# Optimization experiments

Measured on AMD Instinct MI355X. Metric: run time of the kernel, lower is better.

The kernel has to match this reference:

```python
import jax, jax.numpy as jnp
import numpy as np
import math

C = 512
D = C // 4  # 128
SCALE = math.sqrt(D)

def setup_inputs() -> dict:
    key = jax.random.key(0)
    k1, k2, k3, k4 = jax.random.split(key, 4)
    x = jax.random.normal(k1, (8, C, 2048), dtype=jnp.float32)
    # q_conv and k_conv share the same weight (tied in the torch module)
    wqk = jax.random.normal(k2, (D, C), dtype=jnp.float32) * (1.0 / math.sqrt(C))
    wv = jax.random.normal(k3, (D, C), dtype=jnp.float32) * (1.0 / math.sqrt(C))
    bv = jax.random.normal(k4, (D,), dtype=jnp.float32) * 0.01
    return {"x": x, "wqk": wqk, "wv": wv, "bv": bv}

def reference(x, wqk, wv, bv):
    # x: [B, C, N]; 1x1 conv == matmul over channel dim
    xq = jnp.einsum('dc,bcn->bnd', wqk, x)          # [B, N, D]
    xk = jnp.einsum('dc,bcn->bdn', wqk, x)          # [B, D, N]
    xv = jnp.einsum('dc,bcn->bdn', wv, x) + bv[None, :, None]  # [B, D, N]
    energy = jnp.einsum('bnd,bdm->bnm', xq, xk) / SCALE  # [B, N, N]
    attention = jax.nn.softmax(energy, axis=-1)
    x_r = jnp.einsum('bdn,bnm->bdm', xv, attention)  # [B, D, N]
    return x_r
```

## Files before the change

kernel.cpp:

```cpp
#include <hip/hip_runtime.h>

typedef short short4v __attribute__((ext_vector_type(4)));
typedef short short8 __attribute__((ext_vector_type(8)));
typedef float floatx4 __attribute__((ext_vector_type(4)));
typedef unsigned int uint;
typedef unsigned short ushort;

#define CH 512
#define NN 2048
#define DD 128
#define RSCALE 0.08838834764831845f

__device__ __forceinline__ float bf2f(ushort u) {
    union { uint i; float f; } v; v.i = ((uint)u) << 16; return v.f;
}
__device__ __forceinline__ ushort f2bf(float f) {
    union { float f; uint u; } v; v.f = f;
    uint u = v.u;
    return (ushort)((u + 0x7fffu + ((u >> 16) & 1u)) >> 16);
}

__global__ __launch_bounds__(256) void k0_prep(
    const float* __restrict__ wqk, const float* __restrict__ wv,
    ushort* __restrict__ Wbf, float* __restrict__ lsum,
    float* __restrict__ out)
{
    int gid = blockIdx.x * 256 + threadIdx.x;
    float4 z; z.x = 0.f; z.y = 0.f; z.z = 0.f; z.w = 0.f;
    *(float4*)&out[gid * 4] = z;
    if (gid < 32768) {
        int base = gid * 4;
        const float* src = (base < 65536) ? (wqk + base) : (wv + base - 65536);
        float4 v = *(const float4*)src;
        short4v o;
        o[0] = (short)f2bf(v.x); o[1] = (short)f2bf(v.y);
        o[2] = (short)f2bf(v.z); o[3] = (short)f2bf(v.w);
        *(short4v*)&Wbf[base] = o;
    }
    if (gid < 16384) lsum[gid] = 0.0f;
}

__global__ __launch_bounds__(256) void k1_proj(
    const float* __restrict__ x,
    const ushort* __restrict__ Wbf,
    const float* __restrict__ bv,
    ushort* __restrict__ Q,
    ushort* __restrict__ VT)
{
    const int nt = blockIdx.x;
    const int b  = blockIdx.y;
    const int n0 = nt * 32;
    const int t = threadIdx.x;
    const int lane = t & 63, w = t >> 6, l15 = lane & 15, quad = lane >> 4;

    __shared__ __attribute__((aligned(16))) ushort As[32 * 40];
    __shared__ __attribute__((aligned(16))) ushort Bs[256 * 40];
    __shared__ __attribute__((aligned(16))) ushort Vt[128 * 40];

    floatx4 acc[2][4];
#pragma unroll
    for (int i = 0; i < 2; i++)
#pragma unroll
        for (int j = 0; j < 4; j++) acc[i][j] = (floatx4)(0.0f);

    const float* xb = x + b * (CH * NN) + n0;

    for (int c0 = 0; c0 < CH; c0 += 32) {
        {
            int c  = t & 31;
            int ng = t >> 5;
            float4 v = *(const float4*)&xb[(c0 + c) * NN + ng * 4];
            As[(ng * 4 + 0) * 40 + c] = f2bf(v.x);
            As[(ng * 4 + 1) * 40 + c] = f2bf(v.y);
            As[(ng * 4 + 2) * 40 + c] = f2bf(v.z);
            As[(ng * 4 + 3) * 40 + c] = f2bf(v.w);
        }
#pragma unroll
        for (int rep = 0; rep < 4; rep++) {
            int idx = rep * 256 + t;
            int row = idx >> 2, g = idx & 3;
            *(short8*)&Bs[row * 40 + g * 8] = *(const short8*)&Wbf[row * CH + c0 + g * 8];
        }
        __syncthreads();
        short8 a0 = *(short8*)&As[(l15) * 40 + quad * 8];
        short8 a1 = *(short8*)&As[(16 + l15) * 40 + quad * 8];
#pragma unroll
        for (int dt2 = 0; dt2 < 4; dt2++) {
            short8 bf = *(short8*)&Bs[(w * 64 + dt2 * 16 + l15) * 40 + quad * 8];
            acc[0][dt2] = __builtin_amdgcn_mfma_f32_16x16x32_bf16(a0, bf, acc[0][dt2], 0, 0, 0);
            acc[1][dt2] = __builtin_amdgcn_mfma_f32_16x16x32_bf16(a1, bf, acc[1][dt2], 0, 0, 0);
        }
        __syncthreads();
    }

#pragma unroll
    for (int ns = 0; ns < 2; ns++)
#pragma unroll
        for (int dt2 = 0; dt2 < 4; dt2++) {
            int ds_ = w * 64 + dt2 * 16 + l15;
#pragma unroll
            for (int r = 0; r < 4; r++) {
                int nl = ns * 16 + quad * 4 + r;
                float val = acc[ns][dt2][r];
                if (ds_ < 128) {
                    Q[b * (NN * DD) + (n0 + nl) * DD + ds_] = f2bf(val);
                } else {
                    int dv = ds_ - 128;
                    Vt[dv * 40 + nl] = f2bf(val + bv[dv]);
                }
            }
        }
    __syncthreads();
#pragma unroll
    for (int rep = 0; rep < 2; rep++) {
        int idx = rep * 256 + t;
        int dv = idx >> 2, seg = idx & 3;
        *(short8*)&VT[((size_t)b * DD + dv) * NN + n0 + seg * 8] =
            *(short8*)&Vt[dv * 40 + seg * 8];
    }
}

__global__ __launch_bounds__(256) void kl_sum(
    const ushort* __restrict__ Q,
    float* __restrict__ lsum)
{
    int pid = blockIdx.x;
    const int b = blockIdx.y;
    int it = 0;
    while (pid >= (16 - it)) { pid -= (16 - it); it++; }
    const int jt = it + pid;
    const int i0 = it * 128, j0 = jt * 128;
    const int t = threadIdx.x;
    const int lane = t & 63, w = t >> 6, l15 = lane & 15, quad = lane >> 4;
    const int wi = (w >> 1) * 64, wj = (w & 1) * 64;

    __shared__ __attribute__((aligned(16))) ushort Qi[128 * 136];
    __shared__ __attribute__((aligned(16))) ushort Qj[128 * 136];

    const ushort* Qb = Q + b * (NN * DD);

#pragma unroll
    for (int rep = 0; rep < 8; rep++) {
        int idx = rep * 256 + t;
        int row = idx >> 4, g = idx & 15;
        *(short8*)&Qi[row * 136 + g * 8] = *(const short8*)&Qb[(i0 + row) * DD + g * 8];
        *(short8*)&Qj[row * 136 + g * 8] = *(const short8*)&Qb[(j0 + row) * DD + g * 8];
    }
    __syncthreads();

    floatx4 acc[4][4];
#pragma unroll
    for (int i = 0; i < 4; i++)
#pragma unroll
        for (int j = 0; j < 4; j++) acc[i][j] = (floatx4)(0.0f);

#pragma unroll
    for (int kd = 0; kd < 4; kd++) {
        short8 afr[4], bfr[4];
#pragma unroll
        for (int nt = 0; nt < 4; nt++)
            afr[nt] = *(short8*)&Qi[(wi + nt * 16 + l15) * 136 + kd * 32 + quad * 8];
#pragma unroll
        for (int mt = 0; mt < 4; mt++)
            bfr[mt] = *(short8*)&Qj[(wj + mt * 16 + l15) * 136 + kd * 32 + quad * 8];
#pragma unroll
        for (int nt = 0; nt < 4; nt++)
#pragma unroll
            for (int mt = 0; mt < 4; mt++)
                acc[nt][mt] = __builtin_amdgcn_mfma_f32_16x16x32_bf16(afr[nt], bfr[mt], acc[nt][mt], 0, 0, 0);
    }

    float cs[4] = {0.f, 0.f, 0.f, 0.f};
#pragma unroll
    for (int nt = 0; nt < 4; nt++) {
        float rs[4] = {0.f, 0.f, 0.f, 0.f};
#pragma unroll
        for (int mt = 0; mt < 4; mt++)
#pragma unroll
            for (int r = 0; r < 4; r++) {
                float p = __expf(acc[nt][mt][r] * RSCALE);
                rs[r] += p;
                cs[mt] += p;
            }
#pragma unroll
        for (int r = 0; r < 4; r++) {
            float s = rs[r];
            s += __shfl_xor(s, 1);
            s += __shfl_xor(s, 2);
            s += __shfl_xor(s, 4);
            s += __shfl_xor(s, 8);
            if (l15 == 0)
                atomicAdd(&lsum[b * NN + i0 + wi + nt * 16 + quad * 4 + r], s);
        }
    }
    if (it != jt) {
#pragma unroll
        for (int mt = 0; mt < 4; mt++) {
            float s = cs[mt];
            s += __shfl_xor(s, 16);
            s += __shfl_xor(s, 32);
            if (lane < 16)
                atomicAdd(&lsum[b * NN + j0 + wj + mt * 16 + l15], s);
        }
    }
}

__global__ __launch_bounds__(256) void k_fused(
    const ushort* __restrict__ Q,
    const ushort* __restrict__ VT,
    const float* __restrict__ lsum,
    float* __restrict__ out)
{
    const int mt = blockIdx.x;
    const int h  = blockIdx.y;
    const int b  = blockIdx.z;
    const int m0 = mt * 64;
    const int t = threadIdx.x;
    const int lane = t & 63, w = t >> 6, l15 = lane & 15, quad = lane >> 4;

    __shared__ __attribute__((aligned(16))) ushort Qm[64 * 136];
    __shared__ __attribute__((aligned(16))) ushort Qn[64 * 136];
    __shared__ __attribute__((aligned(16))) ushort Vs[128 * 72];
    __shared__ __attribute__((aligned(16))) ushort Ps[64 * 68];

    const ushort* Qb = Q + b * (NN * DD);
    const ushort* VTb = VT + (size_t)b * DD * NN;
    const float* lb = lsum + b * NN;

#pragma unroll
    for (int rep = 0; rep < 4; rep++) {
        int idx = rep * 256 + t;
        int row = idx >> 4, g = idx & 15;
        *(short8*)&Qm[row * 136 + g * 8] = *(const short8*)&Qb[(m0 + row) * DD + g * 8];
    }
    __syncthreads();

    short8 qm[4][4];
#pragma unroll
    for (int ms = 0; ms < 4; ms++)
#pragma unroll
        for (int kd = 0; kd < 4; kd++)
            qm[ms][kd] = *(short8*)&Qm[(ms * 16 + l15) * 136 + kd * 32 + quad * 8];

    floatx4 acc[2][4];
#pragma unroll
    for (int i = 0; i < 2; i++)
#pragma unroll
        for (int j = 0; j < 4; j++) acc[i][j] = (floatx4)(0.0f);

    const int nbeg = h * (NN / 2), nend = nbeg + (NN / 2);
    for (int n0c = nbeg; n0c < nend; n0c += 64) {
        float lw = lb[n0c + w * 16 + l15];
        __syncthreads();
#pragma unroll
        for (int rep = 0; rep < 4; rep++) {
            int idx = rep * 256 + t;
            int row = idx >> 4, g = idx & 15;
            *(short8*)&Qn[row * 136 + g * 8] = *(const short8*)&Qb[(n0c + row) * DD + g * 8];
        }
#pragma unroll
        for (int rep = 0; rep < 4; rep++) {
            int idx = rep * 256 + t;
            int d = idx >> 3, g = idx & 7;
            *(short8*)&Vs[d * 72 + g * 8] = *(const short8*)&VTb[(size_t)d * NN + n0c + g * 8];
        }
        __syncthreads();

        {
            float linv = 1.0f / lw;
            short8 bq[4];
#pragma unroll
            for (int kd = 0; kd < 4; kd++)
                bq[kd] = *(short8*)&Qn[(w * 16 + l15) * 136 + kd * 32 + quad * 8];
#pragma unroll
            for (int ms = 0; ms < 4; ms++) {
                floatx4 s = (floatx4)(0.0f);
#pragma unroll
                for (int kd = 0; kd < 4; kd++)
                    s = __builtin_amdgcn_mfma_f32_16x16x32_bf16(qm[ms][kd], bq[kd], s, 0, 0, 0);
#pragma unroll
                for (int r = 0; r < 4; r++) {
                    float p = __expf(s[r] * RSCALE) * linv;
                    Ps[(ms * 16 + quad * 4 + r) * 68 + w * 16 + l15] = f2bf(p);
                }
            }
        }
        __syncthreads();

#pragma unroll
        for (int kn = 0; kn < 2; kn++) {
            short8 va0 = *(short8*)&Vs[(w * 32 + l15) * 72 + kn * 32 + quad * 8];
            short8 va1 = *(short8*)&Vs[(w * 32 + 16 + l15) * 72 + kn * 32 + quad * 8];
#pragma unroll
            for (int mf = 0; mf < 4; mf++) {
                short8 pb = *(short8*)&Ps[(mf * 16 + l15) * 68 + kn * 32 + quad * 8];
                acc[0][mf] = __builtin_amdgcn_mfma_f32_16x16x32_bf16(va0, pb, acc[0][mf], 0, 0, 0);
                acc[1][mf] = __builtin_amdgcn_mfma_f32_16x16x32_bf16(va1, pb, acc[1][mf], 0, 0, 0);
            }
        }
    }

    float* ob = out + (size_t)b * DD * NN;
#pragma unroll
    for (int dsub = 0; dsub < 2; dsub++)
#pragma unroll
        for (int mf = 0; mf < 4; mf++)
#pragma unroll
            for (int r = 0; r < 4; r++) {
                int d = w * 32 + dsub * 16 + quad * 4 + r;
                atomicAdd(&ob[(size_t)d * NN + m0 + mf * 16 + l15], acc[dsub][mf][r]);
            }
}

__global__ __launch_bounds__(256) void k1_fb(
    const float* __restrict__ x, const float* __restrict__ wqk,
    const float* __restrict__ wv, const float* __restrict__ bv,
    ushort* __restrict__ Q, ushort* __restrict__ V)
{
    const int nt = blockIdx.x;
    const int b  = blockIdx.y;
    const int n0 = nt * 32;
    const int t = threadIdx.x;
    const int lane = t & 63, w = t >> 6, l15 = lane & 15, quad = lane >> 4;

    __shared__ __attribute__((aligned(16))) ushort As[32 * 40];
    __shared__ __attribute__((aligned(16))) ushort Bs[256 * 40];

    floatx4 acc[2][4];
#pragma unroll
    for (int i = 0; i < 2; i++)
#pragma unroll
        for (int j = 0; j < 4; j++) acc[i][j] = (floatx4)(0.0f);

    const float* xb = x + b * (CH * NN) + n0;

    for (int c0 = 0; c0 < CH; c0 += 32) {
        {
            int n = t & 31, g = t >> 5;
            short4v v;
#pragma unroll
            for (int i = 0; i < 4; i++)
                v[i] = (short)f2bf(xb[(c0 + g * 4 + i) * NN + n]);
            *(short4v*)&As[n * 40 + g * 4] = v;
        }
#pragma unroll
        for (int rep = 0; rep < 16; rep++) {
            int idx = rep * 256 + t;
            int row = idx >> 4, cp = idx & 15;
            const float* wf = (row < 128) ? (wqk + row * CH) : (wv + (row - 128) * CH);
            uint pack = (uint)f2bf(wf[c0 + cp * 2]) | ((uint)f2bf(wf[c0 + cp * 2 + 1]) << 16);
            *(uint*)&Bs[row * 40 + cp * 2] = pack;
        }
        __syncthreads();
        short8 a0 = *(short8*)&As[(l15) * 40 + quad * 8];
        short8 a1 = *(short8*)&As[(16 + l15) * 40 + quad * 8];
#pragma unroll
        for (int dt2 = 0; dt2 < 4; dt2++) {
            short8 bf = *(short8*)&Bs[(w * 64 + dt2 * 16 + l15) * 40 + quad * 8];
            acc[0][dt2] = __builtin_amdgcn_mfma_f32_16x16x32_bf16(a0, bf, acc[0][dt2], 0, 0, 0);
            acc[1][dt2] = __builtin_amdgcn_mfma_f32_16x16x32_bf16(a1, bf, acc[1][dt2], 0, 0, 0);
        }
        __syncthreads();
    }
#pragma unroll
    for (int ns = 0; ns < 2; ns++)
#pragma unroll
        for (int dt2 = 0; dt2 < 4; dt2++) {
            int ds_ = w * 64 + dt2 * 16 + l15;
#pragma unroll
            for (int r = 0; r < 4; r++) {
                int n = n0 + ns * 16 + quad * 4 + r;
                float val = acc[ns][dt2][r];
                if (ds_ < 128) {
                    Q[b * (NN * DD) + n * DD + ds_] = f2bf(val);
                } else {
                    int dv = ds_ - 128;
                    V[b * (NN * DD) + n * DD + dv] = f2bf(val + bv[dv]);
                }
            }
        }
}

__global__ __launch_bounds__(256) void k2_norm(
    const ushort* __restrict__ Q, ushort* __restrict__ V)
{
    const int ntile = blockIdx.x;
    const int b = blockIdx.y;
    const int n0 = ntile * 64;
    const int t = threadIdx.x;
    const int lane = t & 63, w = t >> 6, l15 = lane & 15, quad = lane >> 4;

    __shared__ __attribute__((aligned(16))) ushort Qs[64 * 136];
    __shared__ __attribute__((aligned(16))) ushort Qm2[64 * 136];

    const ushort* Qb = Q + b * (NN * DD);

#pragma unroll
    for (int rep = 0; rep < 16; rep++) {
        int idx = rep * 256 + t;
        int row = idx >> 6, dp = idx & 63;
        *(uint*)&Qs[row * 136 + dp * 2] = *(const uint*)&Qb[(n0 + row) * DD + dp * 2];
    }
    __syncthreads();

    short8 afr[4];
#pragma unroll
    for (int kd = 0; kd < 4; kd++)
        afr[kd] = *(short8*)&Qs[(w * 16 + l15) * 136 + kd * 32 + quad * 8];

    float sums[4] = {0.f, 0.f, 0.f, 0.f};

    for (int m0 = 0; m0 < NN; m0 += 64) {
#pragma unroll
        for (int rep = 0; rep < 16; rep++) {
            int idx = rep * 256 + t;
            int row = idx >> 6, dp = idx & 63;
            *(uint*)&Qm2[row * 136 + dp * 2] = *(const uint*)&Qb[(m0 + row) * DD + dp * 2];
        }
        __syncthreads();
#pragma unroll
        for (int ct = 0; ct < 4; ct++) {
            floatx4 s = (floatx4)(0.0f);
#pragma unroll
            for (int kd = 0; kd < 4; kd++) {
                short8 bf = *(short8*)&Qm2[(ct * 16 + l15) * 136 + kd * 32 + quad * 8];
                s = __builtin_amdgcn_mfma_f32_16x16x32_bf16(afr[kd], bf, s, 0, 0, 0);
            }
#pragma unroll
            for (int r = 0; r < 4; r++)
                sums[r] += __expf(s[r] * RSCALE);
        }
        __syncthreads();
    }

#pragma unroll
    for (int r = 0; r < 4; r++) {
        float s = sums[r];
        s += __shfl_xor(s, 1);
        s += __shfl_xor(s, 2);
        s += __shfl_xor(s, 4);
        s += __shfl_xor(s, 8);
        sums[r] = s;
    }

    ushort* Vb = V + b * (NN * DD);
#pragma unroll
    for (int r = 0; r < 4; r++) {
        int n = n0 + w * 16 + quad * 4 + r;
        float inv = 1.0f / sums[r];
        short8 vv = *(short8*)&Vb[n * DD + l15 * 8];
        short8 o;
#pragma unroll
        for (int i = 0; i < 8; i++)
            o[i] = (short)f2bf(bf2f((ushort)vv[i]) * inv);
        *(short8*)&Vb[n * DD + l15 * 8] = o;
    }
}

__global__ __launch_bounds__(256) void k3_attn(
    const ushort* __restrict__ Q, const ushort* __restrict__ Vp,
    float* __restrict__ out)
{
    const int mtile = blockIdx.x;
    const int b = blockIdx.y;
    const int m0 = mtile * 64;
    const int t = threadIdx.x;
    const int lane = t & 63, w = t >> 6, l15 = lane & 15, quad = lane >> 4;

    __shared__ __attribute__((aligned(16))) ushort Qs[64 * 136];
    __shared__ __attribute__((aligned(16))) ushort Qn2[32 * 136];
    __shared__ __attribute__((aligned(16))) ushort Vs2[128 * 40];
    __shared__ __attribute__((aligned(16))) ushort Ps2[64 * 40];

    const ushort* Qb = Q + b * (NN * DD);
    const ushort* Vpb = Vp + b * (NN * DD);

#pragma unroll
    for (int rep = 0; rep < 16; rep++) {
        int idx = rep * 256 + t;
        int row = idx >> 6, dp = idx & 63;
        *(uint*)&Qs[row * 136 + dp * 2] = *(const uint*)&Qb[(m0 + row) * DD + dp * 2];
    }
    __syncthreads();

    short8 afr[4];
#pragma unroll
    for (int kd = 0; kd < 4; kd++)
        afr[kd] = *(short8*)&Qs[(w * 16 + l15) * 136 + kd * 32 + quad * 8];

    floatx4 acc[2][4];
#pragma unroll
    for (int s = 0; s < 2; s++)
#pragma unroll
        for (int mt = 0; mt < 4; mt++) acc[s][mt] = (floatx4)(0.0f);

    for (int n0c = 0; n0c < NN; n0c += 32) {
#pragma unroll
        for (int rep = 0; rep < 8; rep++) {
            int idx = rep * 256 + t;
            int row = idx >> 6, dp = idx & 63;
            *(uint*)&Qn2[row * 136 + dp * 2] = *(const uint*)&Qb[(n0c + row) * DD + dp * 2];
        }
#pragma unroll
        for (int rep = 0; rep < 8; rep++) {
            int idx = rep * 256 + t;
            int np = idx >> 7, d = idx & 127;
            uint v0 = Vpb[(n0c + np * 2) * DD + d];
            uint v1 = Vpb[(n0c + np * 2 + 1) * DD + d];
            *(uint*)&Vs2[d * 40 + np * 2] = v0 | (v1 << 16);
        }
        __syncthreads();

#pragma unroll
        for (int nt2 = 0; nt2 < 2; nt2++) {
            floatx4 s = (floatx4)(0.0f);
#pragma unroll
            for (int kd = 0; kd < 4; kd++) {
                short8 bf = *(short8*)&Qn2[(nt2 * 16 + l15) * 136 + kd * 32 + quad * 8];
                s = __builtin_amdgcn_mfma_f32_16x16x32_bf16(afr[kd], bf, s, 0, 0, 0);
            }
#pragma unroll
            for (int r = 0; r < 4; r++) {
                float p = __expf(s[r] * RSCALE);
                Ps2[(w * 16 + quad * 4 + r) * 40 + nt2 * 16 + l15] = f2bf(p);
            }
        }
        __syncthreads();

        short8 pb[4];
#pragma unroll
        for (int mt = 0; mt < 4; mt++)
            pb[mt] = *(short8*)&Ps2[(mt * 16 + l15) * 40 + quad * 8];
#pragma unroll
        for (int sub = 0; sub < 2; sub++) {
            short8 va = *(short8*)&Vs2[(w * 32 + sub * 16 + l15) * 40 + quad * 8];
#pragma unroll
            for (int mt = 0; mt < 4; mt++)
                acc[sub][mt] = __builtin_amdgcn_mfma_f32_16x16x32_bf16(va, pb[mt], acc[sub][mt], 0, 0, 0);
        }
        __syncthreads();
    }

    float* ob = out + (size_t)b * DD * NN;
#pragma unroll
    for (int sub = 0; sub < 2; sub++)
#pragma unroll
        for (int mt = 0; mt < 4; mt++)
#pragma unroll
            for (int r = 0; r < 4; r++) {
                int d = w * 32 + sub * 16 + quad * 4 + r;
                int m = m0 + mt * 16 + l15;
                ob[(size_t)d * NN + m] = acc[sub][mt][r];
            }
}

extern "C" void kernel_launch(void* const* d_in, const int* in_sizes, int n_in,
                              void* d_out, int out_size, void* d_ws, size_t ws_size,
                              hipStream_t stream) {
    const float* x   = (const float*)d_in[0];
    const float* wqk = (const float*)d_in[1];
    const float* wv  = (const float*)d_in[2];
    const float* bv  = (const float*)d_in[3];
    float* out = (float*)d_out;

    ushort* Q = (ushort*)d_ws;

    if (ws_size >= (size_t)16 * 1024 * 1024) {
        ushort* VT   = (ushort*)((char*)d_ws + (4u << 20));
        ushort* Wbf  = (ushort*)((char*)d_ws + (8u << 20));
        float*  lsum = (float*)((char*)d_ws + (8u << 20) + (256u << 10));

        k0_prep<<<2048, 256, 0, stream>>>(wqk, wv, Wbf, lsum, out);
        k1_proj<<<dim3(64, 8), 256, 0, stream>>>(x, Wbf, bv, Q, VT);
        kl_sum<<<dim3(136, 8), 256, 0, stream>>>(Q, lsum);
        k_fused<<<dim3(32, 2, 8), 256, 0, stream>>>(Q, VT, lsum, out);
    } else {
        ushort* V = (ushort*)((char*)d_ws + (4u << 20));
        k1_fb<<<dim3(64, 8), 256, 0, stream>>>(x, wqk, wv, bv, Q, V);
        k2_norm<<<dim3(32, 8), 256, 0, stream>>>(Q, V);
        k3_attn<<<dim3(32, 8), 256, 0, stream>>>(Q, V, out);
    }
}
```

Measured before the change: 152.5 us.

## Load Q tiles directly to registers, prefetch V, and split N four ways

The fused attention kernel now loads query and key Q fragments straight from global memory into registers, dropping two shared-memory tiles and a barrier. V tile loads are issued into registers before the score and softmax math and written to shared memory afterward, so load latency overlaps compute. The column range is split four ways instead of two, doubling the grid for more occupancy at the cost of more output atomics. The projection kernel's x load is also reorganized to use coalesced scalar reads and a vector LDS store.

```diff
diff --git a/kernel.cpp b/kernel.cpp
--- a/kernel.cpp
+++ b/kernel.cpp
@@ -67,13 +67,12 @@
 
     for (int c0 = 0; c0 < CH; c0 += 32) {
         {
-            int c  = t & 31;
-            int ng = t >> 5;
-            float4 v = *(const float4*)&xb[(c0 + c) * NN + ng * 4];
-            As[(ng * 4 + 0) * 40 + c] = f2bf(v.x);
-            As[(ng * 4 + 1) * 40 + c] = f2bf(v.y);
-            As[(ng * 4 + 2) * 40 + c] = f2bf(v.z);
-            As[(ng * 4 + 3) * 40 + c] = f2bf(v.w);
+            int n = t & 31, g = t >> 5;
+            short4v v;
+#pragma unroll
+            for (int i = 0; i < 4; i++)
+                v[i] = (short)f2bf(xb[(c0 + g * 4 + i) * NN + n]);
+            *(short4v*)&As[n * 40 + g * 4] = v;
         }
 #pragma unroll
         for (int rep = 0; rep < 4; rep++) {
@@ -218,8 +217,6 @@
     const int t = threadIdx.x;
     const int lane = t & 63, w = t >> 6, l15 = lane & 15, quad = lane >> 4;
 
-    __shared__ __attribute__((aligned(16))) ushort Qm[64 * 136];
-    __shared__ __attribute__((aligned(16))) ushort Qn[64 * 136];
     __shared__ __attribute__((aligned(16))) ushort Vs[128 * 72];
     __shared__ __attribute__((aligned(16))) ushort Ps[64 * 68];
 
@@ -227,20 +224,12 @@
     const ushort* VTb = VT + (size_t)b * DD * NN;
     const float* lb = lsum + b * NN;
 
-#pragma unroll
-    for (int rep = 0; rep < 4; rep++) {
-        int idx = rep * 256 + t;
-        int row = idx >> 4, g = idx & 15;
-        *(short8*)&Qm[row * 136 + g * 8] = *(const short8*)&Qb[(m0 + row) * DD + g * 8];
-    }
-    __syncthreads();
-
     short8 qm[4][4];
 #pragma unroll
     for (int ms = 0; ms < 4; ms++)
 #pragma unroll
         for (int kd = 0; kd < 4; kd++)
-            qm[ms][kd] = *(short8*)&Qm[(ms * 16 + l15) * 136 + kd * 32 + quad * 8];
+            qm[ms][kd] = *(const short8*)&Qb[(m0 + ms * 16 + l15) * DD + kd * 32 + quad * 8];
 
     floatx4 acc[2][4];
 #pragma unroll
@@ -248,30 +237,26 @@
 #pragma unroll
         for (int j = 0; j < 4; j++) acc[i][j] = (floatx4)(0.0f);
 
-    const int nbeg = h * (NN / 2), nend = nbeg + (NN / 2);
-    for (int n0c = nbeg; n0c < nend; n0c += 64) {
+    const int nbeg = h * (NN / 4);
+    for (int n0c = nbeg; n0c < nbeg + NN / 4; n0c += 64) {
+        __syncthreads();
+
+        short8 bq[4];
+#pragma unroll
+        for (int kd = 0; kd < 4; kd++)
+            bq[kd] = *(const short8*)&Qb[(n0c + w * 16 + l15) * DD + kd * 32 + quad * 8];
         float lw = lb[n0c + w * 16 + l15];
-        __syncthreads();
+
+        short8 vstage[4];
 #pragma unroll
         for (int rep = 0; rep < 4; rep++) {
             int idx = rep * 256 + t;
-            int row = idx >> 4, g = idx & 15;
-            *(short8*)&Qn[row * 136 + g * 8] = *(const short8*)&Qb[(n0c + row) * DD + g * 8];
-        }
-#pragma unroll
-        for (int rep = 0; rep < 4; rep++) {
-            int idx = rep * 256 + t;
             int d = idx >> 3, g = idx & 7;
-            *(short8*)&Vs[d * 72 + g * 8] = *(const short8*)&VTb[(size_t)d * NN + n0c + g * 8];
-        }
-        __syncthreads();
+            vstage[rep] = *(const short8*)&VTb[(size_t)d * NN + n0c + g * 8];
+        }
 
         {
             float linv = 1.0f / lw;
-            short8 bq[4];
-#pragma unroll
-            for (int kd = 0; kd < 4; kd++)
-                bq[kd] = *(short8*)&Qn[(w * 16 + l15) * 136 + kd * 32 + quad * 8];
 #pragma unroll
             for (int ms = 0; ms < 4; ms++) {
                 floatx4 s = (floatx4)(0.0f);
@@ -284,6 +269,13 @@
                     Ps[(ms * 16 + quad * 4 + r) * 68 + w * 16 + l15] = f2bf(p);
                 }
             }
+        }
+
+#pragma unroll
+        for (int rep = 0; rep < 4; rep++) {
+            int idx = rep * 256 + t;
+            int d = idx >> 3, g = idx & 7;
+            *(short8*)&Vs[d * 72 + g * 8] = vstage[rep];
         }
         __syncthreads();
 
@@ -573,7 +565,7 @@
         k0_prep<<<2048, 256, 0, stream>>>(wqk, wv, Wbf, lsum, out);
         k1_proj<<<dim3(64, 8), 256, 0, stream>>>(x, Wbf, bv, Q, VT);
         kl_sum<<<dim3(136, 8), 256, 0, stream>>>(Q, lsum);
-        k_fused<<<dim3(32, 2, 8), 256, 0, stream>>>(Q, VT, lsum, out);
+        k_fused<<<dim3(32, 4, 8), 256, 0, stream>>>(Q, VT, lsum, out);
     } else {
         ushort* V = (ushort*)((char*)d_ws + (4u << 20));
         k1_fb<<<dim3(64, 8), 256, 0, stream>>>(x, wqk, wv, bv, Q, V);
```

After: 174.8 us. +14.6%, slower.
